# Kernel optimization log

Hardware: AMD Instinct MI355X
Metric: run time of the kernel (lower is better)

## Reference

```python
import jax, jax.numpy as jnp
import numpy as np

N_EMBD = 1024
N_HEAD = 16
HEAD_DIM = N_EMBD // N_HEAD
WINDOW = 256
STRIDE = 128
GLOBAL = 16


def build_sparse_causal_mask(t):
    i = jnp.arange(t)[:, None]
    j = jnp.arange(t)[None, :]
    causal = j <= i
    allowed = causal & ((i - j) < WINDOW)
    allowed = allowed | (((i - j) % STRIDE == 0) & causal)
    allowed = allowed | ((j < GLOBAL) & causal)
    return allowed  # [t, t] bool


def setup_inputs() -> dict:
    key = jax.random.key(0)
    k1, k2, k3, k4, k5 = jax.random.split(key, 5)
    b, t = 2, 4096
    s = 1.0 / np.sqrt(N_EMBD)
    return {
        "x": jax.random.normal(k1, (b, t, N_EMBD), dtype=jnp.float32),
        "w_qkv": jax.random.normal(k2, (N_EMBD, 3 * N_EMBD), dtype=jnp.float32) * s,
        "b_qkv": jnp.zeros((3 * N_EMBD,), dtype=jnp.float32),
        "w_proj": jax.random.normal(k3, (N_EMBD, N_EMBD), dtype=jnp.float32) * s,
        "b_proj": jnp.zeros((N_EMBD,), dtype=jnp.float32),
    }


def reference(x, w_qkv, b_qkv, w_proj, b_proj):
    b, t, c = x.shape
    qkv = x @ w_qkv + b_qkv  # [b, t, 3c]
    q, k, v = jnp.split(qkv, 3, axis=2)
    # [b, h, t, d]
    q = q.reshape(b, t, N_HEAD, HEAD_DIM).transpose(0, 2, 1, 3)
    k = k.reshape(b, t, N_HEAD, HEAD_DIM).transpose(0, 2, 1, 3)
    v = v.reshape(b, t, N_HEAD, HEAD_DIM).transpose(0, 2, 1, 3)

    allowed = build_sparse_causal_mask(t)  # [t, t]
    scale = 1.0 / np.sqrt(HEAD_DIM)
    att = jnp.einsum("bhqd,bhkd->bhqk", q, k) * scale
    att = jnp.where(allowed, att, -jnp.inf)
    att = jax.nn.softmax(att, axis=-1)
    y = jnp.einsum("bhqk,bhkd->bhqd", att, v)
    y = y.transpose(0, 2, 1, 3).reshape(b, t, c)
    return y @ w_proj + b_proj
```

## Files before the change

kernel.cpp:

```cpp
#include <hip/hip_runtime.h>
#include <hip/hip_bf16.h>
#include <stdint.h>

typedef unsigned short ushort_t;
typedef __attribute__((ext_vector_type(8))) __bf16 bf16x8;
typedef __attribute__((ext_vector_type(8))) short short8;
typedef __attribute__((ext_vector_type(4))) float f32x4;
typedef __attribute__((ext_vector_type(4))) unsigned int uint4v;

__device__ __forceinline__ ushort_t f2b(float f) {
  union { float f; uint32_t u; } c; c.f = f;
  return (ushort_t)((c.u + 0x7fffu + ((c.u >> 16) & 1u)) >> 16);
}
__device__ __forceinline__ float b2f(ushort_t b) {
  union { float f; uint32_t u; } c; c.u = ((uint32_t)b) << 16;
  return c.f;
}
__device__ __forceinline__ float dot2bf(uint32_t qu, uint32_t ku, float acc) {
  union { uint32_t u; float f; } a, b, c, d;
  a.u = qu << 16; b.u = qu & 0xffff0000u;
  c.u = ku << 16; d.u = ku & 0xffff0000u;
  acc = fmaf(a.f, c.f, acc);
  return fmaf(b.f, d.f, acc);
}

__global__ __launch_bounds__(256) void f32_to_b16(
    const float* __restrict__ in, ushort_t* __restrict__ out) {
  const int i = (blockIdx.x * 256 + threadIdx.x) * 8;
  const f32x4 a = *(const f32x4*)&in[i];
  const f32x4 b = *(const f32x4*)&in[i + 4];
  short8 t;
#pragma unroll
  for (int j = 0; j < 4; j++) { t[j] = (short)f2b(a[j]); t[4 + j] = (short)f2b(b[j]); }
  *(short8*)&out[i] = t;
}

__global__ __launch_bounds__(256) void transpose_f2b(
    const float* __restrict__ in, ushort_t* __restrict__ out, int K, int N) {
  __shared__ __align__(16) ushort_t tile[64][72];
  const int k0 = blockIdx.x * 64, n0 = blockIdx.y * 64;
  const int tid = threadIdx.x;
#pragma unroll
  for (int i = 0; i < 4; i++) {
    const int idx = i * 256 + tid;
    const int r = idx >> 4, c = (idx & 15) * 4;
    const f32x4 a = *(const f32x4*)&in[(size_t)(k0 + r) * N + n0 + c];
#pragma unroll
    for (int j = 0; j < 4; j++) tile[r][c + j] = f2b(a[j]);
  }
  __syncthreads();
#pragma unroll
  for (int i = 0; i < 16; i++) {
    const int idx = i * 256 + tid;
    const int r = idx >> 6, c = idx & 63;
    out[(size_t)(n0 + r) * K + k0 + c] = tile[c][r];
  }
}

template <int MODE>
__global__ __launch_bounds__(256) void gemm_bt(
    const ushort_t* __restrict__ A, const ushort_t* __restrict__ Bt,
    const float* __restrict__ bias,
    ushort_t* __restrict__ q_out, ushort_t* __restrict__ k_out,
    ushort_t* __restrict__ v_out, float* __restrict__ f_out,
    int M, int N, int K) {
  __shared__ __align__(16) ushort_t Als[128 * 64];
  __shared__ __align__(16) ushort_t Bls[128 * 64];
  const int tid = threadIdx.x;
  const int wave = tid >> 6, lane = tid & 63;
  const int quad = lane >> 4, l15 = lane & 15;
  const int wr = wave >> 1, wc = wave & 1;
  const int rowBase = blockIdx.y * 128;
  const int colBase = blockIdx.x * 128;
  const f32x4 fzero = {0.f, 0.f, 0.f, 0.f};

  f32x4 acc[4][4];
#pragma unroll
  for (int mi = 0; mi < 4; mi++)
#pragma unroll
    for (int ni = 0; ni < 4; ni++) acc[mi][ni] = fzero;

  const int srow = tid >> 3;
  const int scol = (tid & 7) * 8;

  for (int kk = 0; kk < K; kk += 64) {
    __syncthreads();
#pragma unroll
    for (int s = 0; s < 4; s++) {
      const int r = s * 32 + srow;
      *(short8*)&Als[r * 64 + scol] =
          *(const short8*)&A[(size_t)(rowBase + r) * K + kk + scol];
      *(short8*)&Bls[r * 64 + scol] =
          *(const short8*)&Bt[(size_t)(colBase + r) * K + kk + scol];
    }
    __syncthreads();
#pragma unroll
    for (int ks = 0; ks < 2; ks++) {
      const int ko = ks * 32 + quad * 8;
      bf16x8 af[4], bfr[4];
#pragma unroll
      for (int mi = 0; mi < 4; mi++)
        af[mi] = *(const bf16x8*)&Als[(wr * 64 + mi * 16 + l15) * 64 + ko];
#pragma unroll
      for (int ni = 0; ni < 4; ni++)
        bfr[ni] = *(const bf16x8*)&Bls[(wc * 64 + ni * 16 + l15) * 64 + ko];
#pragma unroll
      for (int mi = 0; mi < 4; mi++)
#pragma unroll
        for (int ni = 0; ni < 4; ni++)
          acc[mi][ni] = __builtin_amdgcn_mfma_f32_16x16x32_bf16(
              af[mi], bfr[ni], acc[mi][ni], 0, 0, 0);
    }
  }

  if (MODE == 0) {
    const int which = colBase >> 10;
    ushort_t* dst = which == 0 ? q_out : (which == 1 ? k_out : v_out);
    const int h = ((colBase & 1023) >> 6) + wc;
#pragma unroll
    for (int mi = 0; mi < 4; mi++) {
#pragma unroll
      for (int ni = 0; ni < 4; ni++) {
        const int d = ni * 16 + l15;
        const float bv = bias[colBase + wc * 64 + d];
#pragma unroll
        for (int r = 0; r < 4; r++) {
          const int row = rowBase + wr * 64 + mi * 16 + quad * 4 + r;
          const int bidx = row >> 12, t = row & 4095;
          dst[(size_t)((bidx * 16 + h) * 4096 + t) * 64 + d] =
              f2b(acc[mi][ni][r] + bv);
        }
      }
    }
  } else {
#pragma unroll
    for (int mi = 0; mi < 4; mi++) {
#pragma unroll
      for (int ni = 0; ni < 4; ni++) {
        const int col = colBase + wc * 64 + ni * 16 + l15;
        const float bv = bias[col];
#pragma unroll
        for (int r = 0; r < 4; r++) {
          const int row = rowBase + wr * 64 + mi * 16 + quad * 4 + r;
          f_out[(size_t)row * N + col] = acc[mi][ni][r] + bv;
        }
      }
    }
  }
}

#define LP 72
__global__ __launch_bounds__(256, 3) void sparse_attn(
    const ushort_t* __restrict__ Qb, const ushort_t* __restrict__ Kb,
    const ushort_t* __restrict__ Vb, ushort_t* __restrict__ Y) {
  __shared__ __align__(16) ushort_t Qls[64 * LP];
  __shared__ __align__(16) char smem[(64 * LP + 64 * LP + 4 * 16 * LP) * 2];
  ushort_t* Kls = (ushort_t*)smem;
  ushort_t* Vtls = Kls + 64 * LP;
  ushort_t* Pls = Vtls + 64 * LP;

  const int tid = threadIdx.x;
  const int wave = tid >> 6, lane = tid & 63;
  const int quad = lane >> 4, l15 = lane & 15;
  const int qt = (int)gridDim.x - 1 - (int)blockIdx.x;
  const int h = blockIdx.y, b = blockIdx.z;
  const int q0 = qt * 64;
  const size_t headoff = (size_t)(b * 16 + h) * 4096 * 64;
  const ushort_t* Qp = Qb + headoff;
  const ushort_t* Kp = Kb + headoff;
  const ushort_t* Vp = Vb + headoff;
  const f32x4 fzero = {0.f, 0.f, 0.f, 0.f};
  const float scale = 0.125f;

#pragma unroll
  for (int i = 0; i < 2; i++) {
    const int idx = i * 256 + tid;
    const int r = idx >> 3, c = (idx & 7) * 8;
    *(short8*)&Qls[r * LP + c] = *(const short8*)&Qp[(size_t)(q0 + r) * 64 + c];
  }
  __syncthreads();
  bf16x8 qf[2];
#pragma unroll
  for (int ks = 0; ks < 2; ks++)
    qf[ks] = *(const bf16x8*)&Qls[(wave * 16 + l15) * LP + ks * 32 + quad * 8];

  f32x4 o[4];
#pragma unroll
  for (int dt = 0; dt < 4; dt++) o[dt] = fzero;
  float mrun[4], lsum[4];
#pragma unroll
  for (int r = 0; r < 4; r++) { mrun[r] = -1e30f; lsum[r] = 0.f; }
  ushort_t* Pw = &Pls[wave * 16 * LP];

  auto dense_tile = [&](int k0, int mode) {
    __syncthreads();
#pragma unroll
    for (int i = 0; i < 2; i++) {
      const int idx = i * 256 + tid;
      const int r = idx >> 3, c = (idx & 7) * 8;
      *(short8*)&Kls[r * LP + c] = *(const short8*)&Kp[(size_t)(k0 + r) * 64 + c];
    }
#pragma unroll
    for (int i = 0; i < 2; i++) {
      const int idx = i * 256 + tid;
      const int key = idx & 63, dblk = (idx >> 6) * 8;
      short8 vv = *(const short8*)&Vp[(size_t)(k0 + key) * 64 + dblk];
#pragma unroll
      for (int m = 0; m < 8; m++) Vtls[(dblk + m) * LP + key] = (ushort_t)vv[m];
    }
    __syncthreads();

    f32x4 sacc[4];
#pragma unroll
    for (int ni = 0; ni < 4; ni++) sacc[ni] = fzero;
#pragma unroll
    for (int ks = 0; ks < 2; ks++) {
      const int ko = ks * 32 + quad * 8;
#pragma unroll
      for (int ni = 0; ni < 4; ni++) {
        bf16x8 kf = *(const bf16x8*)&Kls[(ni * 16 + l15) * LP + ko];
        sacc[ni] = __builtin_amdgcn_mfma_f32_16x16x32_bf16(qf[ks], kf, sacc[ni], 0, 0, 0);
      }
    }

    float p[4][4];
    const int i0 = q0 + wave * 16 + quad * 4;
    if (mode == 0) {
#pragma unroll
      for (int ni = 0; ni < 4; ni++)
#pragma unroll
        for (int r = 0; r < 4; r++) p[ni][r] = sacc[ni][r] * scale;
    } else {
#pragma unroll
      for (int ni = 0; ni < 4; ni++) {
        const int j = k0 + ni * 16 + l15;
#pragma unroll
        for (int r = 0; r < 4; r++) {
          const int dist = i0 + r - j;
          bool ok;
          if (mode == 1)      ok = dist >= 0;
          else if (mode == 2) ok = (dist < 256) || ((dist & 127) == 0);
          else                ok = (dist >= 0) &&
                                   ((dist < 256) || ((dist & 127) == 0) || (j < 16));
          p[ni][r] = ok ? sacc[ni][r] * scale : -1e30f;
        }
      }
    }

    float alpha[4];
#pragma unroll
    for (int r = 0; r < 4; r++) {
      float m = fmaxf(fmaxf(p[0][r], p[1][r]), fmaxf(p[2][r], p[3][r]));
      m = fmaxf(m, __shfl_xor(m, 1));
      m = fmaxf(m, __shfl_xor(m, 2));
      m = fmaxf(m, __shfl_xor(m, 4));
      m = fmaxf(m, __shfl_xor(m, 8));
      const float mnew = fmaxf(mrun[r], m);
      alpha[r] = __expf(mrun[r] - mnew);
      mrun[r] = mnew;
      float rs = 0.f;
#pragma unroll
      for (int ni = 0; ni < 4; ni++) {
        const float e = __expf(p[ni][r] - mnew);
        p[ni][r] = e;
        rs += e;
      }
      rs += __shfl_xor(rs, 1);
      rs += __shfl_xor(rs, 2);
      rs += __shfl_xor(rs, 4);
      rs += __shfl_xor(rs, 8);
      lsum[r] = lsum[r] * alpha[r] + rs;
    }
#pragma unroll
    for (int dt = 0; dt < 4; dt++)
#pragma unroll
      for (int r = 0; r < 4; r++) o[dt][r] *= alpha[r];

#pragma unroll
    for (int ni = 0; ni < 4; ni++)
#pragma unroll
      for (int r = 0; r < 4; r++)
        Pw[(quad * 4 + r) * LP + ni * 16 + l15] = f2b(p[ni][r]);
    __syncthreads();

#pragma unroll
    for (int ks = 0; ks < 2; ks++) {
      const int ko = ks * 32 + quad * 8;
      bf16x8 pf = *(const bf16x8*)&Pw[l15 * LP + ko];
#pragma unroll
      for (int dt = 0; dt < 4; dt++) {
        bf16x8 vf = *(const bf16x8*)&Vtls[(dt * 16 + l15) * LP + ko];
        o[dt] = __builtin_amdgcn_mfma_f32_16x16x32_bf16(pf, vf, o[dt], 0, 0, 0);
      }
    }
  };

  if (qt < 6) {
    for (int kt = 0; kt <= qt; kt++) dense_tile(kt * 64, 3);
  } else {
    dense_tile(0, 3);
    dense_tile((qt - 4) * 64, 2);
    dense_tile((qt - 3) * 64, 0);
    dense_tile((qt - 2) * 64, 0);
    dense_tile((qt - 1) * 64, 0);
    dense_tile(qt * 64, 1);

    const int rowl = wave * 16 + l15;
    const uint4v qv0 = *(const uint4v*)&Qls[rowl * LP + quad * 16];
    const uint4v qv1 = *(const uint4v*)&Qls[rowl * LP + quad * 16 + 8];
    const ushort_t* Kr = Kp + (size_t)rowl * 64 + quad * 16;
    const ushort_t* Vr = Vp + (size_t)rowl * 64 + quad * 16;

    float ms = -1e30f, ls = 0.f;
    f32x4 os4[4];
#pragma unroll
    for (int c = 0; c < 4; c++) os4[c] = fzero;

    auto sproc = [&](uint4v ka0, uint4v ka1, uint4v va0, uint4v va1) {
      float sd = 0.f;
#pragma unroll
      for (int m2 = 0; m2 < 4; m2++) {
        sd = dot2bf(qv0[m2], ka0[m2], sd);
        sd = dot2bf(qv1[m2], ka1[m2], sd);
      }
      sd += __shfl_xor(sd, 16);
      sd += __shfl_xor(sd, 32);
      const float sig = sd * scale;
      const float mnew = fmaxf(ms, sig);
      const float al = __expf(ms - mnew);
      const float e = __expf(sig - mnew);
      ms = mnew;
      ls = ls * al + e;
#pragma unroll
      for (int m2 = 0; m2 < 4; m2++) {
        union { uint32_t u; float f; } va, vb, vc, vd;
        va.u = va0[m2] << 16;
        vb.u = va0[m2] & 0xffff0000u;
        vc.u = va1[m2] << 16;
        vd.u = va1[m2] & 0xffff0000u;
        const int d0 = 2 * m2, d1 = 2 * m2 + 1;
        os4[d0 >> 2][d0 & 3] = fmaf(os4[d0 >> 2][d0 & 3], al, e * va.f);
        os4[d1 >> 2][d1 & 3] = fmaf(os4[d1 >> 2][d1 & 3], al, e * vb.f);
        os4[(d0 + 8) >> 2][d0 & 3] = fmaf(os4[(d0 + 8) >> 2][d0 & 3], al, e * vc.f);
        os4[(d1 + 8) >> 2][d1 & 3] = fmaf(os4[(d1 + 8) >> 2][d1 & 3], al, e * vd.f);
      }
    };

    int k0s = q0 - 384;
    if (k0s >= 64) {
      uint4v ka0 = *(const uint4v*)(Kr + (size_t)k0s * 64);
      uint4v ka1 = *(const uint4v*)(Kr + (size_t)k0s * 64 + 8);
      uint4v va0 = *(const uint4v*)(Vr + (size_t)k0s * 64);
      uint4v va1 = *(const uint4v*)(Vr + (size_t)k0s * 64 + 8);
      while (true) {
        const int nxt = k0s - 128;
        uint4v kb0, kb1, vb0, vb1;
        if (nxt >= 64) {
          kb0 = *(const uint4v*)(Kr + (size_t)nxt * 64);
          kb1 = *(const uint4v*)(Kr + (size_t)nxt * 64 + 8);
          vb0 = *(const uint4v*)(Vr + (size_t)nxt * 64);
          vb1 = *(const uint4v*)(Vr + (size_t)nxt * 64 + 8);
        }
        sproc(ka0, ka1, va0, va1);
        if (nxt < 64) break;
        ka0 = kb0; ka1 = kb1; va0 = vb0; va1 = vb1;
        k0s = nxt;
      }
    }

    __syncthreads();
    float* scr = (float*)smem + wave * (16 * 68);
#pragma unroll
    for (int c = 0; c < 4; c++)
      *(f32x4*)&scr[l15 * 68 + quad * 16 + c * 4] = os4[c];
    asm volatile("s_waitcnt lgkmcnt(0)" ::: "memory");
    __builtin_amdgcn_wave_barrier();
#pragma unroll
    for (int r = 0; r < 4; r++) {
      const float ms_r = __shfl(ms, quad * 4 + r);
      const float ls_r = __shfl(ls, quad * 4 + r);
      const float M = fmaxf(mrun[r], ms_r);
      const float ea = __expf(mrun[r] - M);
      const float eb = __expf(ms_r - M);
      lsum[r] = lsum[r] * ea + ls_r * eb;
#pragma unroll
      for (int dt = 0; dt < 4; dt++)
        o[dt][r] = o[dt][r] * ea + scr[(quad * 4 + r) * 68 + dt * 16 + l15] * eb;
    }
  }

#pragma unroll
  for (int dt = 0; dt < 4; dt++) {
#pragma unroll
    for (int r = 0; r < 4; r++) {
      const int t = q0 + wave * 16 + quad * 4 + r;
      const int c = h * 64 + dt * 16 + l15;
      Y[(size_t)(b * 4096 + t) * 1024 + c] = f2b(o[dt][r] / lsum[r]);
    }
  }
}

static const void* by_size(void* const* d_in, const int* in_sizes, int n_in,
                           int want, int fallback_idx) {
  for (int i = 0; i < n_in; i++)
    if (in_sizes[i] == want) return d_in[i];
  return d_in[fallback_idx];
}

extern "C" void kernel_launch(void* const* d_in, const int* in_sizes, int n_in,
                              void* d_out, int out_size, void* d_ws,
                              size_t ws_size, hipStream_t stream) {
  const float* x      = (const float*)by_size(d_in, in_sizes, n_in, 8388608, 0);
  const float* w_qkv  = (const float*)by_size(d_in, in_sizes, n_in, 3145728, 1);
  const float* b_qkv  = (const float*)by_size(d_in, in_sizes, n_in, 3072, 2);
  const float* w_proj = (const float*)by_size(d_in, in_sizes, n_in, 1048576, 3);
  const float* b_proj = (const float*)by_size(d_in, in_sizes, n_in, 1024, 4);
  float* out = (float*)d_out;
  char* ws = (char*)d_ws;
  ushort_t* wqkvT  = (ushort_t*)(ws);
  ushort_t* wprojT = (ushort_t*)(ws + 6291456);
  ushort_t* qb     = (ushort_t*)(ws + 8388608);
  ushort_t* kb     = (ushort_t*)(ws + 25165824);
  ushort_t* vb     = (ushort_t*)(ws + 41943040);
  ushort_t* yb     = (ushort_t*)(ws + 58720256);
  ushort_t* xb     = yb;

  if (ws_size < 75497472) return;

  f32_to_b16<<<4096, 256, 0, stream>>>(x, xb);
  transpose_f2b<<<dim3(16, 48), 256, 0, stream>>>(w_qkv, wqkvT, 1024, 3072);
  transpose_f2b<<<dim3(16, 16), 256, 0, stream>>>(w_proj, wprojT, 1024, 1024);
  gemm_bt<0><<<dim3(24, 64), 256, 0, stream>>>(
      xb, wqkvT, b_qkv, qb, kb, vb, nullptr, 8192, 3072, 1024);
  sparse_attn<<<dim3(64, 16, 2), 256, 0, stream>>>(qb, kb, vb, yb);
  gemm_bt<1><<<dim3(8, 64), 256, 0, stream>>>(
      yb, wprojT, b_proj, nullptr, nullptr, nullptr, out, 8192, 1024, 1024);
}
```

Baseline: 367.2 us.

## Raise attention occupancy, remap blocks per XCD, use direct global-to-LDS GEMM loads

The attention kernel drops the Q shared-memory staging and loads Q fragments straight from global memory. It shrinks LDS row padding from 72 to 68 and raises the launch bound from 3 to 5 blocks per CU. It also remaps the linear block index so each XCD works on a few head pairs, removes a block-wide barrier before the P·V MFMAs (P is private to each wave), and splits the strided dot product into two accumulators. The GEMM stages its A and B tiles with global_load_lds instead of going through registers. These changes target LDS footprint, barrier stalls and L2 locality. The risks are register spills at the higher occupancy bound and misaligned 16-byte LDS reads, since a 68-element stride gives 136-byte rows.

Result: slower. 389.4 us (+6.0%).

```diff
diff --git a/kernel.cpp b/kernel.cpp
--- a/kernel.cpp
+++ b/kernel.cpp
@@ -88,10 +88,16 @@
 #pragma unroll
     for (int s = 0; s < 4; s++) {
       const int r = s * 32 + srow;
-      *(short8*)&Als[r * 64 + scol] =
-          *(const short8*)&A[(size_t)(rowBase + r) * K + kk + scol];
-      *(short8*)&Bls[r * 64 + scol] =
-          *(const short8*)&Bt[(size_t)(colBase + r) * K + kk + scol];
+      __builtin_amdgcn_global_load_lds(
+          (const __attribute__((address_space(1))) unsigned int*)
+              &A[(size_t)(rowBase + r) * K + kk + scol],
+          (__attribute__((address_space(3))) unsigned int*)&Als[r * 64 + scol],
+          16, 0, 0);
+      __builtin_amdgcn_global_load_lds(
+          (const __attribute__((address_space(1))) unsigned int*)
+              &Bt[(size_t)(colBase + r) * K + kk + scol],
+          (__attribute__((address_space(3))) unsigned int*)&Bls[r * 64 + scol],
+          16, 0, 0);
     }
     __syncthreads();
 #pragma unroll
@@ -149,40 +155,41 @@
   }
 }
 
-#define LP 72
-__global__ __launch_bounds__(256, 3) void sparse_attn(
+#define LP2 68
+__global__ __launch_bounds__(256, 5) void sparse_attn(
     const ushort_t* __restrict__ Qb, const ushort_t* __restrict__ Kb,
     const ushort_t* __restrict__ Vb, ushort_t* __restrict__ Y) {
-  __shared__ __align__(16) ushort_t Qls[64 * LP];
-  __shared__ __align__(16) char smem[(64 * LP + 64 * LP + 4 * 16 * LP) * 2];
-  ushort_t* Kls = (ushort_t*)smem;
-  ushort_t* Vtls = Kls + 64 * LP;
-  ushort_t* Pls = Vtls + 64 * LP;
+  __shared__ __align__(16) ushort_t KVls[2 * 64 * LP2];
+  __shared__ __align__(16) ushort_t Pls[4 * 16 * LP2];
+  ushort_t* Kls = KVls;
+  ushort_t* Vtls = KVls + 64 * LP2;
 
   const int tid = threadIdx.x;
   const int wave = tid >> 6, lane = tid & 63;
   const int quad = lane >> 4, l15 = lane & 15;
-  const int qt = (int)gridDim.x - 1 - (int)blockIdx.x;
-  const int h = blockIdx.y, b = blockIdx.z;
+
+  const int linear = (int)blockIdx.x + 64 * (int)blockIdx.y + 1024 * (int)blockIdx.z;
+  const int xcd = linear & 7, slot = linear >> 3;
+  const int pair = xcd * 4 + (slot >> 6);
+  const int qt = 63 - (slot & 63);
+  const int h = pair & 15, b = pair >> 4;
   const int q0 = qt * 64;
-  const size_t headoff = (size_t)(b * 16 + h) * 4096 * 64;
+  const size_t headoff = (size_t)pair * 4096 * 64;
   const ushort_t* Qp = Qb + headoff;
   const ushort_t* Kp = Kb + headoff;
   const ushort_t* Vp = Vb + headoff;
   const f32x4 fzero = {0.f, 0.f, 0.f, 0.f};
   const float scale = 0.125f;
-
-#pragma unroll
-  for (int i = 0; i < 2; i++) {
-    const int idx = i * 256 + tid;
-    const int r = idx >> 3, c = (idx & 7) * 8;
-    *(short8*)&Qls[r * LP + c] = *(const short8*)&Qp[(size_t)(q0 + r) * 64 + c];
-  }
-  __syncthreads();
+  const int rowl = wave * 16 + l15;
+
   bf16x8 qf[2];
-#pragma unroll
-  for (int ks = 0; ks < 2; ks++)
-    qf[ks] = *(const bf16x8*)&Qls[(wave * 16 + l15) * LP + ks * 32 + quad * 8];
+  qf[0] = *(const bf16x8*)&Qp[(size_t)(q0 + rowl) * 64 + quad * 8];
+  qf[1] = *(const bf16x8*)&Qp[(size_t)(q0 + rowl) * 64 + 32 + quad * 8];
+  uint4v qv0 = {0u, 0u, 0u, 0u}, qv1 = {0u, 0u, 0u, 0u};
+  if (q0 >= 448) {
+    qv0 = *(const uint4v*)&Qp[(size_t)(q0 + rowl) * 64 + quad * 16];
+    qv1 = *(const uint4v*)&Qp[(size_t)(q0 + rowl) * 64 + quad * 16 + 8];
+  }
 
   f32x4 o[4];
 #pragma unroll
@@ -190,7 +197,7 @@
   float mrun[4], lsum[4];
 #pragma unroll
   for (int r = 0; r < 4; r++) { mrun[r] = -1e30f; lsum[r] = 0.f; }
-  ushort_t* Pw = &Pls[wave * 16 * LP];
+  ushort_t* Pw = &Pls[wave * 16 * LP2];
 
   auto dense_tile = [&](int k0, int mode) {
     __syncthreads();
@@ -198,7 +205,7 @@
     for (int i = 0; i < 2; i++) {
       const int idx = i * 256 + tid;
       const int r = idx >> 3, c = (idx & 7) * 8;
-      *(short8*)&Kls[r * LP + c] = *(const short8*)&Kp[(size_t)(k0 + r) * 64 + c];
+      *(short8*)&Kls[r * LP2 + c] = *(const short8*)&Kp[(size_t)(k0 + r) * 64 + c];
     }
 #pragma unroll
     for (int i = 0; i < 2; i++) {
@@ -206,7 +213,7 @@
       const int key = idx & 63, dblk = (idx >> 6) * 8;
       short8 vv = *(const short8*)&Vp[(size_t)(k0 + key) * 64 + dblk];
 #pragma unroll
-      for (int m = 0; m < 8; m++) Vtls[(dblk + m) * LP + key] = (ushort_t)vv[m];
+      for (int m = 0; m < 8; m++) Vtls[(dblk + m) * LP2 + key] = (ushort_t)vv[m];
     }
     __syncthreads();
 
@@ -218,7 +225,7 @@
       const int ko = ks * 32 + quad * 8;
 #pragma unroll
       for (int ni = 0; ni < 4; ni++) {
-        bf16x8 kf = *(const bf16x8*)&Kls[(ni * 16 + l15) * LP + ko];
+        bf16x8 kf = *(const bf16x8*)&Kls[(ni * 16 + l15) * LP2 + ko];
         sacc[ni] = __builtin_amdgcn_mfma_f32_16x16x32_bf16(qf[ks], kf, sacc[ni], 0, 0, 0);
       }
     }
@@ -280,16 +287,15 @@
     for (int ni = 0; ni < 4; ni++)
 #pragma unroll
       for (int r = 0; r < 4; r++)
-        Pw[(quad * 4 + r) * LP + ni * 16 + l15] = f2b(p[ni][r]);
-    __syncthreads();
+        Pw[(quad * 4 + r) * LP2 + ni * 16 + l15] = f2b(p[ni][r]);
 
 #pragma unroll
     for (int ks = 0; ks < 2; ks++) {
       const int ko = ks * 32 + quad * 8;
-      bf16x8 pf = *(const bf16x8*)&Pw[l15 * LP + ko];
+      bf16x8 pf = *(const bf16x8*)&Pw[l15 * LP2 + ko];
 #pragma unroll
       for (int dt = 0; dt < 4; dt++) {
-        bf16x8 vf = *(const bf16x8*)&Vtls[(dt * 16 + l15) * LP + ko];
+        bf16x8 vf = *(const bf16x8*)&Vtls[(dt * 16 + l15) * LP2 + ko];
         o[dt] = __builtin_amdgcn_mfma_f32_16x16x32_bf16(pf, vf, o[dt], 0, 0, 0);
       }
     }
@@ -305,9 +311,6 @@
     dense_tile((qt - 1) * 64, 0);
     dense_tile(qt * 64, 1);
 
-    const int rowl = wave * 16 + l15;
-    const uint4v qv0 = *(const uint4v*)&Qls[rowl * LP + quad * 16];
-    const uint4v qv1 = *(const uint4v*)&Qls[rowl * LP + quad * 16 + 8];
     const ushort_t* Kr = Kp + (size_t)rowl * 64 + quad * 16;
     const ushort_t* Vr = Vp + (size_t)rowl * 64 + quad * 16;
 
@@ -317,12 +320,13 @@
     for (int c = 0; c < 4; c++) os4[c] = fzero;
 
     auto sproc = [&](uint4v ka0, uint4v ka1, uint4v va0, uint4v va1) {
-      float sd = 0.f;
+      float sa = 0.f, sb = 0.f;
 #pragma unroll
       for (int m2 = 0; m2 < 4; m2++) {
-        sd = dot2bf(qv0[m2], ka0[m2], sd);
-        sd = dot2bf(qv1[m2], ka1[m2], sd);
-      }
+        sa = dot2bf(qv0[m2], ka0[m2], sa);
+        sb = dot2bf(qv1[m2], ka1[m2], sb);
+      }
+      float sd = sa + sb;
       sd += __shfl_xor(sd, 16);
       sd += __shfl_xor(sd, 32);
       const float sig = sd * scale;
@@ -369,7 +373,7 @@
     }
 
     __syncthreads();
-    float* scr = (float*)smem + wave * (16 * 68);
+    float* scr = (float*)KVls + wave * (16 * 68);
 #pragma unroll
     for (int c = 0; c < 4; c++)
       *(f32x4*)&scr[l15 * 68 + quad * 16 + c * 4] = os4[c];
```
